# Performance work log

Measured on AMD Instinct MI355X. Metric: run time of the kernel, lower is better.

## Reference

```python
import jax, jax.numpy as jnp
import numpy as np

B, S, D = 2, 4096, 512
H, DK, DV = 8, 64, 64
LN_EPS = 1e-5
ATTN_EPS = 1e-6


def layer_norm(x, g, b):
    mu = jnp.mean(x, axis=-1, keepdims=True)
    var = jnp.var(x, axis=-1, keepdims=True)
    return (x - mu) * jax.lax.rsqrt(var + LN_EPS) * g + b


def setup_inputs() -> dict:
    key = jax.random.key(0)
    ks = jax.random.split(key, 12)
    s = 1.0 / np.sqrt(D)
    inp = {
        "Q": jax.random.normal(ks[0], (B, S, D), jnp.float32),
        "K": jax.random.normal(ks[1], (B, S, D), jnp.float32),
        "V": jax.random.normal(ks[2], (B, S, D), jnp.float32),
        "W_q": jax.random.normal(ks[3], (D, H * DK), jnp.float32) * s,
        "W_k": jax.random.normal(ks[4], (D, H * DK), jnp.float32) * s,
        "W_v": jax.random.normal(ks[5], (D, H * DV), jnp.float32) * s,
        "W_o": jax.random.normal(ks[6], (H * DV, D), jnp.float32) * s,
        "ln1_g": jnp.ones((D,), jnp.float32),
        "ln1_b": jnp.zeros((D,), jnp.float32),
        "ln2_g": jnp.ones((D,), jnp.float32),
        "ln2_b": jnp.zeros((D,), jnp.float32),
        "w1": jax.random.normal(ks[7], (4 * D, D), jnp.float32) * s,  # torch Linear: (out, in)
        "b1": jnp.zeros((4 * D,), jnp.float32),
        "w2": jax.random.normal(ks[8], (D, 4 * D), jnp.float32) * (1.0 / np.sqrt(4 * D)),
        "b2": jnp.zeros((D,), jnp.float32),
    }
    return inp


def reference(Q, K, V, W_q, W_k, W_v, W_o, ln1_g, ln1_b, ln2_g, ln2_b, w1, b1, w2, b2):
    Qn = layer_norm(Q, ln1_g, ln1_b)
    # project and split heads: [B,S,H,dk] -> [B,H,S,dk]
    q = (Qn @ W_q).reshape(B, S, H, DK).transpose(0, 2, 1, 3)
    k = (K @ W_k).reshape(B, S, H, DK).transpose(0, 2, 1, 3)
    v = (V @ W_v).reshape(B, S, H, DV).transpose(0, 2, 1, 3)
    scores = jnp.einsum("bhqd,bhkd->bhqk", q, k) / (np.sqrt(DK) + ATTN_EPS)
    attn = jax.nn.softmax(scores, axis=-1)  # same as max-subtract softmax
    ctx = jnp.einsum("bhqk,bhkd->bhqd", attn, v)
    ctx = ctx.transpose(0, 2, 1, 3).reshape(B, S, H * DV)
    att_out = ctx @ W_o  # dropout = identity (eval)
    X = Q + att_out
    Xn = layer_norm(X, ln2_g, ln2_b)
    h = jax.nn.gelu(Xn @ w1.T + b1, approximate=False)
    ffn = h @ w2.T + b2
    return X + ffn
```

## Files before the change

### kernel.cpp

```cpp
#include <hip/hip_runtime.h>

typedef unsigned short u16;
typedef __attribute__((ext_vector_type(8))) short short8;
typedef __attribute__((ext_vector_type(4))) float f32x4;
typedef __attribute__((ext_vector_type(16))) float f32x16;
typedef __attribute__((ext_vector_type(4))) unsigned u32x4;

struct __align__(8) us4 { u16 x, y, z, w; };
struct __align__(8) ui2 { unsigned x, y; };

#define CEXP (1.44269504089f / (8.0f + 1e-6f))

__device__ __forceinline__ u16 f2bf(float f) {
  unsigned u = __builtin_bit_cast(unsigned, f);
  unsigned r = (u + 0x7FFFu + ((u >> 16) & 1u)) >> 16;
  return (u16)r;
}

__device__ __forceinline__ unsigned pack_bf2_trunc(float a, float b) {
  return __builtin_amdgcn_perm(__builtin_bit_cast(unsigned, b),
                               __builtin_bit_cast(unsigned, a), 0x07060302u);
}

__device__ __forceinline__ void async_load16(const void* g, void* l) {
  __builtin_amdgcn_global_load_lds((const __attribute__((address_space(1))) void*)g,
                                   (__attribute__((address_space(3))) void*)l, 16, 0, 0);
}

__global__ void prep_weights(const float* __restrict__ Wq, const float* __restrict__ Wk,
                             const float* __restrict__ Wv, const float* __restrict__ Wo,
                             const float* __restrict__ w1, const float* __restrict__ w2,
                             u16* __restrict__ wqkvT, u16* __restrict__ woT,
                             u16* __restrict__ w1b, u16* __restrict__ w2b) {
  const int z = blockIdx.y;
  const int stride = gridDim.x * blockDim.x;
  const int i0 = blockIdx.x * blockDim.x + threadIdx.x;
  if (z < 4) {
    const float* src = z == 0 ? Wq : z == 1 ? Wk : z == 2 ? Wv : Wo;
    u16* dst = z < 3 ? wqkvT + z * 512 * 512 : woT;
    const float scale = (z == 0) ? CEXP : 1.0f;
    for (int i = i0; i < 512 * 512; i += stride) {
      int n = i >> 9, k = i & 511;
      dst[i] = f2bf(src[k * 512 + n] * scale);
    }
  } else {
    const float* src = z == 4 ? w1 : w2;
    u16* dst = z == 4 ? w1b : w2b;
    for (int i = i0; i < 2048 * 512; i += stride) dst[i] = f2bf(src[i]);
  }
}

template <bool KV>
__launch_bounds__(128)
__global__ void ln_cast(const float* __restrict__ X, const float* __restrict__ gw,
                        const float* __restrict__ bw, u16* __restrict__ Y,
                        const float* __restrict__ Kin, const float* __restrict__ Vin,
                        u16* __restrict__ Kb, u16* __restrict__ Vb) {
  const int row = blockIdx.x, t = threadIdx.x;
  const size_t base = (size_t)row * 512;
  float4 x = ((const float4*)(X + base))[t];
  float s = x.x + x.y + x.z + x.w;
  float ss = x.x * x.x + x.y * x.y + x.z * x.z + x.w * x.w;
#pragma unroll
  for (int off = 32; off > 0; off >>= 1) {
    s += __shfl_xor(s, off);
    ss += __shfl_xor(ss, off);
  }
  __shared__ float red[4];
  if ((t & 63) == 0) { red[(t >> 6) * 2] = s; red[(t >> 6) * 2 + 1] = ss; }
  __syncthreads();
  const float tot = red[0] + red[2], tss = red[1] + red[3];
  const float mu = tot * (1.0f / 512.0f);
  const float var = tss * (1.0f / 512.0f) - mu * mu;
  const float rs = rsqrtf(var + 1e-5f);
  float4 g4 = ((const float4*)gw)[t];
  float4 b4 = ((const float4*)bw)[t];
  us4 o;
  o.x = f2bf((x.x - mu) * rs * g4.x + b4.x);
  o.y = f2bf((x.y - mu) * rs * g4.y + b4.y);
  o.z = f2bf((x.z - mu) * rs * g4.z + b4.z);
  o.w = f2bf((x.w - mu) * rs * g4.w + b4.w);
  ((us4*)(Y + base))[t] = o;
  if constexpr (KV) {
    float4 k4 = ((const float4*)(Kin + base))[t];
    float4 v4 = ((const float4*)(Vin + base))[t];
    us4 ko, vo;
    ko.x = f2bf(k4.x); ko.y = f2bf(k4.y); ko.z = f2bf(k4.z); ko.w = f2bf(k4.w);
    vo.x = f2bf(v4.x); vo.y = f2bf(v4.y); vo.z = f2bf(v4.z); vo.w = f2bf(v4.w);
    ((us4*)(Kb + base))[t] = ko;
    ((us4*)(Vb + base))[t] = vo;
  }
}

__launch_bounds__(256, 3)
__global__ void gemm_qkv(const u16* __restrict__ Aq, const u16* __restrict__ Ak,
                         const u16* __restrict__ Av, const u16* __restrict__ Bt,
                         u16* __restrict__ qb, u16* __restrict__ kb, u16* __restrict__ vtb) {
  __shared__ __align__(16) u16 sA[2][128 * 32];
  __shared__ __align__(16) u16 sB[2][128 * 32];
  const int tid = threadIdx.x;
  const int wave = tid >> 6, lane = tid & 63;
  const int l15 = lane & 15, quad = lane >> 4;
  const int qsw = (quad ^ ((l15 >> 1) & 3)) * 8;
  const int m0 = blockIdx.x * 128, n0 = blockIdx.y * 128;
  const int sel = n0 >> 9;
  const u16* A = sel == 0 ? Aq : sel == 1 ? Ak : Av;
  const int wm = (wave >> 1) * 64, wn = (wave & 1) * 64;
  const int u0 = wave * 64 + lane, u1 = u0 + 256;
  const int sw0 = ((u0 & 3) ^ ((u0 >> 3) & 3)) * 8;
  const int K = 512;

  const u16* a0 = A + (size_t)(m0 + (u0 >> 2)) * K + sw0;
  const u16* a1 = A + (size_t)(m0 + (u1 >> 2)) * K + sw0;
  const u16* b0 = Bt + (size_t)(n0 + (u0 >> 2)) * K + sw0;
  const u16* b1p = Bt + (size_t)(n0 + (u1 >> 2)) * K + sw0;

  f32x4 acc[4][4] = {};
  for (int k0 = 0; k0 < K; k0 += 64) {
#pragma unroll
    for (int hf = 0; hf < 2; hf++) {
      const int kk = k0 + hf * 32;
      async_load16(a0 + kk, &sA[hf][wave * 512]);
      async_load16(a1 + kk, &sA[hf][2048 + wave * 512]);
      async_load16(b0 + kk, &sB[hf][wave * 512]);
      async_load16(b1p + kk, &sB[hf][2048 + wave * 512]);
    }
    __syncthreads();
#pragma unroll
    for (int hf = 0; hf < 2; hf++) {
      short8 af[4], bfr[4];
#pragma unroll
      for (int i = 0; i < 4; i++)
        af[i] = *(const short8*)&sA[hf][(wm + i * 16 + l15) * 32 + qsw];
#pragma unroll
      for (int j = 0; j < 4; j++)
        bfr[j] = *(const short8*)&sB[hf][(wn + j * 16 + l15) * 32 + qsw];
#pragma unroll
      for (int i = 0; i < 4; i++)
#pragma unroll
        for (int j = 0; j < 4; j++)
          acc[i][j] = __builtin_amdgcn_mfma_f32_16x16x32_bf16(af[i], bfr[j], acc[i][j], 0, 0, 0);
    }
    __syncthreads();
  }

#pragma unroll
  for (int i = 0; i < 4; i++) {
#pragma unroll
    for (int j = 0; j < 4; j++) {
      const int ocol = ((n0 + wn) & 511) + j * 16 + l15;
      const int row0 = m0 + wm + i * 16 + quad * 4;
      if (sel == 0) {
#pragma unroll
        for (int r = 0; r < 4; r++) qb[(size_t)(row0 + r) * 512 + ocol] = f2bf(acc[i][j][r]);
      } else if (sel == 1) {
        const int d = ocol & 63, hh2 = ocol >> 6;
        const int ks = d >> 4, hik = (d >> 3) & 1, e = d & 7;
#pragma unroll
        for (int r = 0; r < 4; r++) {
          const int row = row0 + r;
          const int bb = row >> 12, keys = row & 4095;
          const size_t addr =
              (((size_t)((bb * 8 + hh2) * 128 + (keys >> 5)) * 4 + ks) * 64 +
               (keys & 31) + 32 * hik) * 8 + e;
          kb[addr] = f2bf(acc[i][j][r]);
        }
      } else {
        const int b = row0 >> 12, s0 = row0 & 4095;
        const int hh = ocol >> 6, cc = ocol & 63;
        us4 pk;
        pk.x = f2bf(acc[i][j][0]); pk.y = f2bf(acc[i][j][1]);
        pk.z = f2bf(acc[i][j][2]); pk.w = f2bf(acc[i][j][3]);
        *(us4*)&vtb[((size_t)((b * 8 + hh) * 64 + cc) << 12) + s0] = pk;
      }
    }
  }
}

template <int EP, int TN, int LB>
__launch_bounds__(256, LB)
__global__ void gemm_bt(const u16* __restrict__ A, const u16* __restrict__ Bt,
                        int M, int N, int K, void* __restrict__ Cp,
                        const float* __restrict__ bias, const float* __restrict__ res) {
  constexpr int MI = (TN == 128) ? 4 : 2;
  __shared__ __align__(16) u16 sA[2][128 * 32];
  __shared__ __align__(16) u16 sB[2][TN * 32];
  const int tid = threadIdx.x;
  const int wave = tid >> 6, lane = tid & 63;
  const int l15 = lane & 15, quad = lane >> 4;
  const int qsw = (quad ^ ((l15 >> 1) & 3)) * 8;
  const int m0 = blockIdx.x * 128, n0 = blockIdx.y * TN;
  const int wm = (TN == 128) ? (wave >> 1) * 64 : wave * 32;
  const int wn = (TN == 128) ? (wave & 1) * 64 : 0;
  const int u0 = wave * 64 + lane, u1 = u0 + 256;
  const int sw0 = ((u0 & 3) ^ ((u0 >> 3) & 3)) * 8;

  const u16* a0 = A + (size_t)(m0 + (u0 >> 2)) * K + sw0;
  const u16* a1 = A + (size_t)(m0 + (u1 >> 2)) * K + sw0;
  const u16* b0 = Bt + (size_t)(n0 + (u0 >> 2)) * K + sw0;

  f32x4 acc[MI][4] = {};
  for (int k0 = 0; k0 < K; k0 += 64) {
#pragma unroll
    for (int hf = 0; hf < 2; hf++) {
      const int kk = k0 + hf * 32;
      async_load16(a0 + kk, &sA[hf][wave * 512]);
      async_load16(a1 + kk, &sA[hf][2048 + wave * 512]);
      async_load16(b0 + kk, &sB[hf][wave * 512]);
      if constexpr (TN == 128) {
        const u16* b1p = Bt + (size_t)(n0 + (u1 >> 2)) * K + sw0;
        async_load16(b1p + kk, &sB[hf][2048 + wave * 512]);
      }
    }
    __syncthreads();
#pragma unroll
    for (int hf = 0; hf < 2; hf++) {
      short8 af[MI], bfr[4];
#pragma unroll
      for (int i = 0; i < MI; i++)
        af[i] = *(const short8*)&sA[hf][(wm + i * 16 + l15) * 32 + qsw];
#pragma unroll
      for (int j = 0; j < 4; j++)
        bfr[j] = *(const short8*)&sB[hf][(wn + j * 16 + l15) * 32 + qsw];
#pragma unroll
      for (int i = 0; i < MI; i++)
#pragma unroll
        for (int j = 0; j < 4; j++)
          acc[i][j] = __builtin_amdgcn_mfma_f32_16x16x32_bf16(af[i], bfr[j], acc[i][j], 0, 0, 0);
    }
    __syncthreads();
  }

#pragma unroll
  for (int i = 0; i < MI; i++) {
#pragma unroll
    for (int j = 0; j < 4; j++) {
      const int col = n0 + wn + j * 16 + l15;
      const int row0 = m0 + wm + i * 16 + quad * 4;
      if (EP == 2) {
        float* C = (float*)Cp;
#pragma unroll
        for (int r = 0; r < 4; r++) {
          size_t idx = (size_t)(row0 + r) * N + col;
          C[idx] = acc[i][j][r] + res[idx];
        }
      } else if (EP == 3) {
        u16* C = (u16*)Cp;
        const float bv = bias[col];
#pragma unroll
        for (int r = 0; r < 4; r++) {
          float xx = acc[i][j][r] + bv;
          float gl = 0.5f * xx * (1.0f + erff(xx * 0.70710678118f));
          C[(size_t)(row0 + r) * N + col] = f2bf(gl);
        }
      } else {
        float* C = (float*)Cp;
        const float bv = bias[col];
#pragma unroll
        for (int r = 0; r < 4; r++) {
          size_t idx = (size_t)(row0 + r) * N + col;
          C[idx] = acc[i][j][r] + bv + res[idx];
        }
      }
    }
  }
}

__launch_bounds__(512, 2)
__global__ void attn_kernel(const u16* __restrict__ qb, const u16* __restrict__ kfrag,
                            const u16* __restrict__ vtb, u16* __restrict__ ctx) {
  __shared__ __align__(16) u16 smem[16896];
  const int tid = threadIdx.x;
  const int wave = tid >> 6, lane = tid & 63;
  const int l31 = lane & 31, hi = lane >> 5;
  const int qg = wave >> 1, kh = wave & 1;
  const int bh = blockIdx.x, b = bh >> 3, h = bh & 7;
  const int q0 = blockIdx.y * 128;
  const size_t rb = (size_t)b * 4096;
  const int qrow = q0 + qg * 32 + l31;

  short8 qf[4];
#pragma unroll
  for (int ks = 0; ks < 4; ks++)
    qf[ks] = *(const short8*)&qb[(rb + qrow) * 512 + h * 64 + ks * 16 + hi * 8];

  int voff[2][2];
#pragma unroll
  for (int vb = 0; vb < 2; vb++) {
    const int vrow = vb * 32 + l31;
    voff[vb][0] = vrow * 64 + (((kh * 4 + hi) ^ (vrow & 7))) * 8;
    voff[vb][1] = vrow * 64 + (((kh * 4 + 2 + hi) ^ (vrow & 7))) * 8;
  }

  const int srow = tid >> 3, ssl = (tid & 7) ^ (srow & 7);
  const u16* vp = vtb + (size_t)(bh * 64 + srow) * 4096 + ssl * 8;
  const int sdst = tid * 8;

  const u16* kp = kfrag + ((size_t)(bh * 128 + kh) * 4) * 512 + lane * 8;

  short8 kc[4];
  f32x16 ov[2] = {};
  float l_part = 0.f;

  async_load16(vp, &smem[sdst]);
  vp += 64;
  asm volatile("" ::: "memory");
#pragma unroll
  for (int ks = 0; ks < 4; ks++) kc[ks] = *(const short8*)(kp + ks * 512);
  kp += 4096;
  asm volatile("s_waitcnt vmcnt(4)" ::: "memory");
  __builtin_amdgcn_s_barrier();

#define BODY(VB, COND)                                                              \
  {                                                                                 \
    f32x16 st = {};                                                                 \
    __builtin_amdgcn_s_setprio(1);                                                  \
    _Pragma("unroll") for (int ks = 0; ks < 4; ks++)                                \
      st = __builtin_amdgcn_mfma_f32_32x32x16_bf16(kc[ks], qf[ks], st, 0, 0, 0);    \
    __builtin_amdgcn_s_setprio(0);                                                  \
    if (COND) {                                                                     \
      async_load16(vp, &smem[(1 - (VB)) * 4096 + sdst]);                            \
      vp += 64;                                                                     \
      asm volatile("" ::: "memory");                                                \
      _Pragma("unroll") for (int ks = 0; ks < 4; ks++)                              \
        kc[ks] = *(const short8*)(kp + ks * 512);                                   \
      kp += 4096;                                                                   \
    }                                                                               \
    float p[16];                                                                    \
    _Pragma("unroll") for (int i = 0; i < 16; i++)                                  \
        p[i] = __builtin_amdgcn_exp2f(st[i]);                                       \
    _Pragma("unroll") for (int i = 0; i < 16; i += 4)                               \
        l_part += (p[i] + p[i + 1]) + (p[i + 2] + p[i + 3]);                        \
    unsigned x0 = pack_bf2_trunc(p[0], p[1]), x1 = pack_bf2_trunc(p[2], p[3]);      \
    unsigned x2 = pack_bf2_trunc(p[4], p[5]), x3 = pack_bf2_trunc(p[6], p[7]);      \
    unsigned x4 = pack_bf2_trunc(p[8], p[9]), x5 = pack_bf2_trunc(p[10], p[11]);    \
    unsigned x6 = pack_bf2_trunc(p[12], p[13]), x7 = pack_bf2_trunc(p[14], p[15]);  \
    auto r0 = __builtin_amdgcn_permlane32_swap(x0, x2, false, false);               \
    auto r1 = __builtin_amdgcn_permlane32_swap(x1, x3, false, false);               \
    auto r2 = __builtin_amdgcn_permlane32_swap(x4, x6, false, false);               \
    auto r3 = __builtin_amdgcn_permlane32_swap(x5, x7, false, false);               \
    u32x4 w0 = {r0[0], r1[0], r0[1], r1[1]};                                        \
    u32x4 w1 = {r2[0], r3[0], r2[1], r3[1]};                                        \
    short8 pf0 = __builtin_bit_cast(short8, w0);                                    \
    short8 pf1 = __builtin_bit_cast(short8, w1);                                    \
    __builtin_amdgcn_s_setprio(1);                                                  \
    _Pragma("unroll") for (int vb = 0; vb < 2; vb++) {                              \
      short8 vf0 = *(const short8*)&smem[(VB) * 4096 + voff[vb][0]];                \
      short8 vf1 = *(const short8*)&smem[(VB) * 4096 + voff[vb][1]];                \
      ov[vb] = __builtin_amdgcn_mfma_f32_32x32x16_bf16(vf0, pf0, ov[vb], 0, 0, 0);  \
      ov[vb] = __builtin_amdgcn_mfma_f32_32x32x16_bf16(vf1, pf1, ov[vb], 0, 0, 0);  \
    }                                                                               \
    __builtin_amdgcn_s_setprio(0);                                                  \
    if (COND) {                                                                     \
      asm volatile("s_waitcnt vmcnt(4)" ::: "memory");                              \
      __builtin_amdgcn_s_barrier();                                                 \
    }                                                                               \
  }

  for (int g = 0; g < 32; g++) {
    BODY(0, true);
    BODY(1, (g < 31));
  }
#undef BODY

  float l2 = l_part + __shfl_xor(l_part, 32);
  __syncthreads();
  float* mrg = (float*)smem;
  float* mrgl = (float*)smem + 8192;
  if (kh == 1) {
#pragma unroll
    for (int vb = 0; vb < 2; vb++)
#pragma unroll
      for (int e = 0; e < 16; e++)
        mrg[(qg * 32 + vb * 16 + e) * 64 + lane] = ov[vb][e];
    mrgl[qg * 64 + lane] = l2;
  }
  __syncthreads();
  if (kh == 0) {
    const float inv = 1.0f / (l2 + mrgl[qg * 64 + lane]);
#pragma unroll
    for (int vb = 0; vb < 2; vb++) {
#pragma unroll
      for (int rg = 0; rg < 4; rg++) {
        us4 o;
        o.x = f2bf((ov[vb][rg * 4 + 0] + mrg[(qg * 32 + vb * 16 + rg * 4 + 0) * 64 + lane]) * inv);
        o.y = f2bf((ov[vb][rg * 4 + 1] + mrg[(qg * 32 + vb * 16 + rg * 4 + 1) * 64 + lane]) * inv);
        o.z = f2bf((ov[vb][rg * 4 + 2] + mrg[(qg * 32 + vb * 16 + rg * 4 + 2) * 64 + lane]) * inv);
        o.w = f2bf((ov[vb][rg * 4 + 3] + mrg[(qg * 32 + vb * 16 + rg * 4 + 3) * 64 + lane]) * inv);
        *(us4*)&ctx[(rb + qrow) * 512 + h * 64 + vb * 32 + rg * 8 + hi * 4] = o;
      }
    }
  }
}

extern "C" void kernel_launch(void* const* d_in, const int* in_sizes, int n_in,
                              void* d_out, int out_size, void* d_ws, size_t ws_size,
                              hipStream_t stream) {
  (void)in_sizes; (void)n_in; (void)out_size; (void)ws_size;
  const float* Q = (const float*)d_in[0];
  const float* K = (const float*)d_in[1];
  const float* V = (const float*)d_in[2];
  const float* W_q = (const float*)d_in[3];
  const float* W_k = (const float*)d_in[4];
  const float* W_v = (const float*)d_in[5];
  const float* W_o = (const float*)d_in[6];
  const float* ln1_g = (const float*)d_in[7];
  const float* ln1_b = (const float*)d_in[8];
  const float* ln2_g = (const float*)d_in[9];
  const float* ln2_b = (const float*)d_in[10];
  const float* w1 = (const float*)d_in[11];
  const float* b1 = (const float*)d_in[12];
  const float* w2 = (const float*)d_in[13];
  const float* b2 = (const float*)d_in[14];

  char* w = (char*)d_ws;
  const size_t MB = 1u << 20;
  u16* wqkvT = (u16*)(w);
  u16* woT = (u16*)(w + 3 * MB / 2);
  u16* w1b = (u16*)(w + 2 * MB);
  u16* w2b = (u16*)(w + 4 * MB);
  u16* Qn  = (u16*)(w + 6 * MB);
  u16* Kb  = (u16*)(w + 14 * MB);
  u16* Vb  = (u16*)(w + 22 * MB);
  u16* qb  = (u16*)(w + 30 * MB);
  u16* kb  = (u16*)(w + 38 * MB);
  u16* vtb = (u16*)(w + 46 * MB);
  u16* ctx = (u16*)(w + 54 * MB);
  float* X = (float*)(w + 62 * MB);
  u16* Xn  = (u16*)(w + 6 * MB);
  u16* hb  = (u16*)(w + 14 * MB);

  prep_weights<<<dim3(128, 6), 256, 0, stream>>>(W_q, W_k, W_v, W_o, w1, w2,
                                                 wqkvT, woT, w1b, w2b);
  ln_cast<true><<<8192, 128, 0, stream>>>(Q, ln1_g, ln1_b, Qn, K, V, Kb, Vb);
  gemm_qkv<<<dim3(64, 12), 256, 0, stream>>>(Qn, Kb, Vb, wqkvT, qb, kb, vtb);
  attn_kernel<<<dim3(16, 32), 512, 0, stream>>>(qb, kb, vtb, ctx);
  gemm_bt<2, 64, 3><<<dim3(64, 8), 256, 0, stream>>>(ctx, woT, 8192, 512, 512, X, nullptr, Q);
  ln_cast<false><<<8192, 128, 0, stream>>>(X, ln2_g, ln2_b, Xn, nullptr, nullptr, nullptr, nullptr);
  gemm_bt<3, 128, 3><<<dim3(64, 16), 256, 0, stream>>>(Xn, w1b, 8192, 2048, 512, hb, b1, nullptr);
  gemm_bt<4, 64, 3><<<dim3(64, 8), 256, 0, stream>>>(hb, w2b, 8192, 512, 2048, (float*)d_out, b2, X);
}
```

Baseline: 311.1 us.

## Software-pipeline QK MFMA one tile ahead of softmax in attention; raise occupancy bounds

The attention inner loop is restructured so the QK^T MFMA for the next key tile is issued while exp2 and the PV MFMAs of the current tile run, using two ping-ponged score accumulators. The K fragment prefetch and waitcnt/barrier logic are adjusted for the new prologue and tail. Separately, launch bounds (min blocks per CU) are raised from 3 to 4 for the QKV and other GEMMs. Together these aim to hide MFMA and exp latency and to increase occupancy, at the cost of extra registers that could cause spills.

```diff
diff --git a/kernel.cpp b/kernel.cpp
--- a/kernel.cpp
+++ b/kernel.cpp
@@ -92,7 +92,7 @@
   }
 }
 
-__launch_bounds__(256, 3)
+__launch_bounds__(256, 4)
 __global__ void gemm_qkv(const u16* __restrict__ Aq, const u16* __restrict__ Ak,
                          const u16* __restrict__ Av, const u16* __restrict__ Bt,
                          u16* __restrict__ qb, u16* __restrict__ kb, u16* __restrict__ vtb) {
@@ -299,6 +299,7 @@
   const u16* kp = kfrag + ((size_t)(bh * 128 + kh) * 4) * 512 + lane * 8;
 
   short8 kc[4];
+  f32x16 stA, stB;
   f32x16 ov[2] = {};
   float l_part = 0.f;
 
@@ -308,29 +309,42 @@
 #pragma unroll
   for (int ks = 0; ks < 4; ks++) kc[ks] = *(const short8*)(kp + ks * 512);
   kp += 4096;
-  asm volatile("s_waitcnt vmcnt(4)" ::: "memory");
+  asm volatile("s_waitcnt vmcnt(0)" ::: "memory");
   __builtin_amdgcn_s_barrier();
-
-#define BODY(VB, COND)                                                              \
+  stA = (f32x16){};
+  __builtin_amdgcn_s_setprio(1);
+#pragma unroll
+  for (int ks = 0; ks < 4; ks++)
+    stA = __builtin_amdgcn_mfma_f32_32x32x16_bf16(kc[ks], qf[ks], stA, 0, 0, 0);
+  __builtin_amdgcn_s_setprio(0);
+#pragma unroll
+  for (int ks = 0; ks < 4; ks++) kc[ks] = *(const short8*)(kp + ks * 512);
+  kp += 4096;
+
+#define STEP(T, VB, CUR, NXT)                                                       \
   {                                                                                 \
-    f32x16 st = {};                                                                 \
-    __builtin_amdgcn_s_setprio(1);                                                  \
-    _Pragma("unroll") for (int ks = 0; ks < 4; ks++)                                \
-      st = __builtin_amdgcn_mfma_f32_32x32x16_bf16(kc[ks], qf[ks], st, 0, 0, 0);    \
-    __builtin_amdgcn_s_setprio(0);                                                  \
-    if (COND) {                                                                     \
+    if ((T) < 63) {                                                                 \
       async_load16(vp, &smem[(1 - (VB)) * 4096 + sdst]);                            \
       vp += 64;                                                                     \
       asm volatile("" ::: "memory");                                                \
+    }                                                                               \
+    float p[16];                                                                    \
+    _Pragma("unroll") for (int i = 0; i < 16; i++)                                  \
+        p[i] = __builtin_amdgcn_exp2f((CUR)[i]);                                    \
+    _Pragma("unroll") for (int i = 0; i < 16; i += 4)                               \
+        l_part += (p[i] + p[i + 1]) + (p[i + 2] + p[i + 3]);                        \
+    if ((T) < 63) {                                                                 \
+      (NXT) = (f32x16){};                                                           \
+      __builtin_amdgcn_s_setprio(1);                                                \
+      _Pragma("unroll") for (int ks = 0; ks < 4; ks++)                              \
+        (NXT) = __builtin_amdgcn_mfma_f32_32x32x16_bf16(kc[ks], qf[ks], (NXT), 0, 0, 0); \
+      __builtin_amdgcn_s_setprio(0);                                                \
+    }                                                                               \
+    if ((T) < 62) {                                                                 \
       _Pragma("unroll") for (int ks = 0; ks < 4; ks++)                              \
         kc[ks] = *(const short8*)(kp + ks * 512);                                   \
       kp += 4096;                                                                   \
     }                                                                               \
-    float p[16];                                                                    \
-    _Pragma("unroll") for (int i = 0; i < 16; i++)                                  \
-        p[i] = __builtin_amdgcn_exp2f(st[i]);                                       \
-    _Pragma("unroll") for (int i = 0; i < 16; i += 4)                               \
-        l_part += (p[i] + p[i + 1]) + (p[i + 2] + p[i + 3]);                        \
     unsigned x0 = pack_bf2_trunc(p[0], p[1]), x1 = pack_bf2_trunc(p[2], p[3]);      \
     unsigned x2 = pack_bf2_trunc(p[4], p[5]), x3 = pack_bf2_trunc(p[6], p[7]);      \
     unsigned x4 = pack_bf2_trunc(p[8], p[9]), x5 = pack_bf2_trunc(p[10], p[11]);    \
@@ -351,17 +365,20 @@
       ov[vb] = __builtin_amdgcn_mfma_f32_32x32x16_bf16(vf1, pf1, ov[vb], 0, 0, 0);  \
     }                                                                               \
     __builtin_amdgcn_s_setprio(0);                                                  \
-    if (COND) {                                                                     \
-      asm volatile("s_waitcnt vmcnt(4)" ::: "memory");                              \
+    if ((T) < 63) {                                                                 \
+      if ((T) < 62)                                                                 \
+        asm volatile("s_waitcnt vmcnt(4)" ::: "memory");                            \
+      else                                                                          \
+        asm volatile("s_waitcnt vmcnt(0)" ::: "memory");                            \
       __builtin_amdgcn_s_barrier();                                                 \
     }                                                                               \
   }
 
   for (int g = 0; g < 32; g++) {
-    BODY(0, true);
-    BODY(1, (g < 31));
-  }
-#undef BODY
+    STEP(2 * g, 0, stA, stB);
+    STEP(2 * g + 1, 1, stB, stA);
+  }
+#undef STEP
 
   float l2 = l_part + __shfl_xor(l_part, 32);
   __syncthreads();
@@ -435,8 +452,8 @@
   ln_cast<true><<<8192, 128, 0, stream>>>(Q, ln1_g, ln1_b, Qn, K, V, Kb, Vb);
   gemm_qkv<<<dim3(64, 12), 256, 0, stream>>>(Qn, Kb, Vb, wqkvT, qb, kb, vtb);
   attn_kernel<<<dim3(16, 32), 512, 0, stream>>>(qb, kb, vtb, ctx);
-  gemm_bt<2, 64, 3><<<dim3(64, 8), 256, 0, stream>>>(ctx, woT, 8192, 512, 512, X, nullptr, Q);
+  gemm_bt<2, 64, 4><<<dim3(64, 8), 256, 0, stream>>>(ctx, woT, 8192, 512, 512, X, nullptr, Q);
   ln_cast<false><<<8192, 128, 0, stream>>>(X, ln2_g, ln2_b, Xn, nullptr, nullptr, nullptr, nullptr);
-  gemm_bt<3, 128, 3><<<dim3(64, 16), 256, 0, stream>>>(Xn, w1b, 8192, 2048, 512, hb, b1, nullptr);
-  gemm_bt<4, 64, 3><<<dim3(64, 8), 256, 0, stream>>>(hb, w2b, 8192, 512, 2048, (float*)d_out, b2, X);
-}
+  gemm_bt<3, 128, 4><<<dim3(64, 16), 256, 0, stream>>>(Xn, w1b, 8192, 2048, 512, hb, b1, nullptr);
+  gemm_bt<4, 64, 4><<<dim3(64, 8), 256, 0, stream>>>(hb, w2b, 8192, 512, 2048, (float*)d_out, b2, X);
+}
```

New measurement: 310.1 us. No clear change (-0.3%).
